# Performance work log

Measured on AMD Instinct MI355X. Metric: run time of the kernel, lower is better.

## Reference

```python
import jax, jax.numpy as jnp
import numpy as np

B = 2048      # env batch (graphs)
A = 8         # agents per graph (fully connected)
N = B * A     # total nodes
DIN = 192     # raw obs dim
HD = 256      # h_dim (base MLP)
MD = 256      # mem_dim (GRU)
GD = 128      # gnn_dim (per-head GATv2 out, concat=False -> head mean)
H = 4         # GAT heads
NA = 20       # n_actions
ED = 3        # edge_dim


def setup_inputs() -> dict:
    key = jax.random.key(0)
    ks = jax.random.split(key, 16)
    # fully-connected directed graph per group of A agents, no self loops
    s, d = np.meshgrid(np.arange(A), np.arange(A), indexing='ij')
    mask = s != d
    s = s[mask]; d = d[mask]                     # [A*(A-1)]
    off = (np.arange(B) * A)[:, None]
    src = (off + s[None, :]).reshape(-1)
    dst = (off + d[None, :]).reshape(-1)
    edge_index = jnp.asarray(np.stack([src, dst]), dtype=jnp.int32)  # [2, E]
    E = src.shape[0]
    p = lambda k, sh: jax.random.normal(ks[k], sh, jnp.float32) * 0.02
    return {
        'inputs': jax.random.normal(ks[0], (N, DIN), jnp.float32),
        'hidden_states': jax.random.normal(ks[1], (N, MD), jnp.float32) * 0.1,
        'edge_index': edge_index,
        'edge_attr': jax.random.uniform(ks[2], (E, ED), jnp.float32),
        # base MLP (2 layers: Linear+ReLU+LayerNorm)
        'W1': p(3, (DIN, HD)), 'b1': jnp.zeros(HD), 'g1': jnp.ones(HD), 'be1': jnp.zeros(HD),
        'W2': p(4, (HD, HD)),  'b2': jnp.zeros(HD), 'g2': jnp.ones(HD), 'be2': jnp.zeros(HD),
        # GRUCell
        'Wih': p(5, (3 * MD, HD)), 'Whh': p(6, (3 * MD, MD)),
        'bih': jnp.zeros(3 * MD), 'bhh': jnp.zeros(3 * MD),
        # GATv2Conv (edge_dim=3, heads=4, concat=False, residual)
        'Wl': p(7, (MD, H * GD)), 'bl': jnp.zeros(H * GD),
        'Wr': p(8, (MD, H * GD)), 'br': jnp.zeros(H * GD),
        'att': p(9, (H, GD)),
        'We': p(10, (ED, H * GD)),
        'Wres': p(11, (MD, GD)),
        'bg': jnp.zeros(GD),
        # head: LayerNorm + Linear
        'lng': jnp.ones(GD), 'lnb': jnp.zeros(GD),
        'Wout': p(12, (GD, NA)), 'bout': jnp.zeros(NA),
    }


def _ln(x, g, b):
    mu = jnp.mean(x, -1, keepdims=True)
    xc = x - mu
    v = jnp.mean(xc * xc, -1, keepdims=True)
    return xc * jax.lax.rsqrt(v + 1e-5) * g + b


def _fwd(inputs, hidden_states, edge_attr, edge_index,
         W1, b1, g1, be1, W2, b2, g2, be2,
         Wih, Whh, bih, bhh,
         Wl, bl, Wr, br, att, We, Wres, bg,
         lng, lnb, Wout, bout):
    src, dst = edge_index[0], edge_index[1]
    # ---- base MLP encode ----
    x = _ln(jax.nn.relu(inputs @ W1 + b1), g1, be1)
    x = _ln(jax.nn.relu(x @ W2 + b2), g2, be2)          # [N, HD]
    # ---- SimpleConv(aggr='mean', combine_root='self_loop') ----
    s = jax.ops.segment_sum(x[src], dst, num_segments=N) + x
    deg = jax.ops.segment_sum(jnp.ones(src.shape[0], x.dtype), dst, num_segments=N) + 1.0
    x = s / deg[:, None]                                 # [N, HD]
    # ---- GRUCell ----
    gi = x @ Wih.T + bih
    gh = hidden_states @ Whh.T + bhh
    ir, iz, inn = jnp.split(gi, 3, -1)
    hr, hz, hn = jnp.split(gh, 3, -1)
    r = jax.nn.sigmoid(ir + hr)
    z = jax.nn.sigmoid(iz + hz)
    n = jnp.tanh(inn + r * hn)
    h = (1.0 - z) * n + z * hidden_states                # [N, MD]
    # ---- GATv2Conv (add self loops, edge_attr fill='mean') ----
    loop = jnp.arange(N, dtype=src.dtype)
    sf = jnp.concatenate([src, loop])
    df = jnp.concatenate([dst, loop])
    ea = jnp.concatenate([edge_attr, jnp.broadcast_to(edge_attr.mean(0), (N, ED))], 0)
    xl = (h @ Wl + bl).reshape(N, H, GD)
    xr = (h @ Wr + br).reshape(N, H, GD)
    m = xl[sf] + xr[df] + (ea @ We).reshape(-1, H, GD)   # [Ef, H, GD]
    m = jnp.where(m > 0, m, 0.2 * m)                     # leaky_relu(0.2)
    logits = jnp.einsum('ehc,hc->eh', m, att)            # [Ef, H]
    mx = jax.ops.segment_max(logits, df, num_segments=N)
    ex = jnp.exp(logits - mx[df])
    den = jax.ops.segment_sum(ex, df, num_segments=N)
    alpha = ex / (den[df] + 1e-16)                       # segment softmax
    out = jax.ops.segment_sum(xl[sf] * alpha[..., None], df, num_segments=N)
    out = out.mean(1) + h @ Wres + bg                    # head mean + residual + bias
    zg = jax.nn.relu(out)                                # [N, GD]
    # ---- action head ----
    q = _ln(zg, lng, lnb) @ Wout + bout                  # [N, NA]
    return q, h


def reference(inputs, hidden_states, edge_index, edge_attr,
              W1, b1, g1, be1, W2, b2, g2, be2,
              Wih, Whh, bih, bhh,
              Wl, bl, Wr, br, att, We, Wres, bg,
              lng, lnb, Wout, bout):
    return _fwd(inputs, hidden_states, edge_attr, edge_index,
                W1, b1, g1, be1, W2, b2, g2, be2,
                Wih, Whh, bih, bhh,
                Wl, bl, Wr, br, att, We, Wres, bg,
                lng, lnb, Wout, bout)
```

## Files before the change

### kernel.cpp

```cpp
#include <hip/hip_runtime.h>
#include <hip/hip_bf16.h>

constexpr int NB  = 2048;
constexpr int AG  = 8;
constexpr int NN  = NB * AG;
constexpr int DIN = 192;
constexpr int HD  = 256;
constexpr int MD  = 256;
constexpr int GD  = 128;
constexpr int NA  = 20;
constexpr int NE  = NB * AG * (AG - 1);

typedef __attribute__((ext_vector_type(8))) short bfrag8;
typedef __attribute__((ext_vector_type(4))) short sfrag4;
typedef __attribute__((ext_vector_type(4))) float f32x4;

#define MFMA16(a, b, c) __builtin_amdgcn_mfma_f32_16x16x32_bf16((a), (b), (c), 0, 0, 0)

__device__ __forceinline__ float bf2f(__hip_bfloat16 x) { return __bfloat162float(x); }
__device__ __forceinline__ __hip_bfloat16 f2bf(float x) { return __float2bfloat16(x); }
__device__ __forceinline__ short f2bs(float x) {
    __hip_bfloat16 b = __float2bfloat16(x);
    return *reinterpret_cast<short*>(&b);
}
__device__ __forceinline__ bfrag8 ldf(const __hip_bfloat16* p) { return *(const bfrag8*)p; }
__device__ __forceinline__ bfrag8 ldf32(const float* p) {
    const f32x4 a = *(const f32x4*)p;
    const f32x4 b = *(const f32x4*)(p + 4);
    bfrag8 r;
    r[0] = f2bs(a[0]); r[1] = f2bs(a[1]); r[2] = f2bs(a[2]); r[3] = f2bs(a[3]);
    r[4] = f2bs(b[0]); r[5] = f2bs(b[1]); r[6] = f2bs(b[2]); r[7] = f2bs(b[3]);
    return r;
}
__device__ __forceinline__ float sigmf(float x) { return 1.f / (1.f + __expf(-x)); }
__device__ __forceinline__ float blo(unsigned u) { return __uint_as_float(u << 16); }
__device__ __forceinline__ float bhi(unsigned u) { return __uint_as_float(u & 0xffff0000u); }

__global__ __launch_bounds__(256) void k_prep(
    const float* __restrict__ W1, const float* __restrict__ W2,
    const float* __restrict__ Wih, const float* __restrict__ Whh,
    const float* __restrict__ Wl, const float* __restrict__ bl,
    const float* __restrict__ Wr, const float* __restrict__ br,
    const float* __restrict__ Wres, const float* __restrict__ Wout,
    const float* __restrict__ ea,
    __hip_bfloat16* __restrict__ W1T, __hip_bfloat16* __restrict__ W2T,
    __hip_bfloat16* __restrict__ WihB, __hip_bfloat16* __restrict__ WhhB,
    __hip_bfloat16* __restrict__ WcatT, float* __restrict__ WoutTf,
    float* __restrict__ bcat, float* __restrict__ ea_partials)
{
    __shared__ float sw[4][3];
    const int tid = threadIdx.x;
    if (blockIdx.x >= 3151) {
        const int b = blockIdx.x - 3151;
        float a0 = 0.f, a1 = 0.f, a2 = 0.f;
#pragma unroll
        for (int k = 0; k < 7; k++) {
            int e = b * 1792 + k * 256 + tid;
            a0 += ea[e * 3 + 0];
            a1 += ea[e * 3 + 1];
            a2 += ea[e * 3 + 2];
        }
#pragma unroll
        for (int off = 1; off < 64; off <<= 1) {
            a0 += __shfl_xor(a0, off); a1 += __shfl_xor(a1, off); a2 += __shfl_xor(a2, off);
        }
        if ((tid & 63) == 0) { sw[tid >> 6][0] = a0; sw[tid >> 6][1] = a1; sw[tid >> 6][2] = a2; }
        __syncthreads();
        if (tid == 0) {
            ea_partials[b * 3 + 0] = sw[0][0] + sw[1][0] + sw[2][0] + sw[3][0];
            ea_partials[b * 3 + 1] = sw[0][1] + sw[1][1] + sw[2][1] + sw[3][1];
            ea_partials[b * 3 + 2] = sw[0][2] + sw[1][2] + sw[2][2] + sw[3][2];
        }
        return;
    }
    int i = blockIdx.x * 256 + tid;
    if (i < 49152) { int o = i / 192, c = i % 192; W1T[i] = f2bf(W1[c * 256 + o]); return; }
    i -= 49152;
    if (i < 65536) { int o = i >> 8, c = i & 255; W2T[i] = f2bf(W2[c * 256 + o]); return; }
    i -= 65536;
    if (i < 196608) { WihB[i] = f2bf(Wih[i]); return; }
    i -= 196608;
    if (i < 196608) { WhhB[i] = f2bf(Whh[i]); return; }
    i -= 196608;
    if (i < 294912) {
        int o = i >> 8, c = i & 255;
        float v;
        if (o < 512)       v = Wl[c * 512 + o];
        else if (o < 1024) v = Wr[c * 512 + (o - 512)];
        else               v = Wres[c * 128 + (o - 1024)];
        WcatT[i] = f2bf(v); return;
    }
    i -= 294912;
    if (i < 2560) { int o = i >> 7, c = i & 127; WoutTf[i] = Wout[c * 20 + o]; return; }
    i -= 2560;
    if (i < 1152) {
        float v = 0.f;
        if (i < 512) v = bl[i]; else if (i < 1024) v = br[i - 512];
        bcat[i] = v;
    }
}

__global__ __launch_bounds__(256) void k_encode(
    const float* __restrict__ in,
    const __hip_bfloat16* __restrict__ W1T,
    const float* __restrict__ b1, const float* __restrict__ g1, const float* __restrict__ be1,
    const __hip_bfloat16* __restrict__ W2T,
    const float* __restrict__ b2, const float* __restrict__ g2, const float* __restrict__ be2,
    __hip_bfloat16* __restrict__ xm)
{
    __shared__ float sf[16][257];
    __shared__ alignas(16) __hip_bfloat16 sb[16][264];
    const int tid = threadIdx.x;
    const int lane = tid & 63, w = tid >> 6;
    const int r = lane & 15, q = lane >> 4;
    const int m0 = blockIdx.x * 16;

    {
        bfrag8 af[6];
        const float* ap = in + (size_t)(m0 + r) * DIN + q * 8;
#pragma unroll
        for (int kb = 0; kb < 6; kb++) af[kb] = ldf32(ap + kb * 32);
#pragma unroll
        for (int i = 0; i < 4; i++) {
            int t = w * 4 + i;
            const __hip_bfloat16* wp = W1T + (size_t)(t * 16 + r) * DIN + q * 8;
            bfrag8 bf[6];
#pragma unroll
            for (int kb = 0; kb < 6; kb++) bf[kb] = ldf(wp + kb * 32);
            f32x4 acc = (f32x4){0.f, 0.f, 0.f, 0.f};
#pragma unroll
            for (int kb = 0; kb < 6; kb++) acc = MFMA16(af[kb], bf[kb], acc);
            int col = t * 16 + r;
            float bias = b1[col];
#pragma unroll
            for (int reg = 0; reg < 4; reg++)
                sf[q * 4 + reg][col] = fmaxf(acc[reg] + bias, 0.f);
        }
    }
    __syncthreads();
    {
        int rowi = tid >> 4, c16 = tid & 15;
        float vals[16]; float s = 0.f, s2 = 0.f;
#pragma unroll
        for (int j = 0; j < 16; j++) { float v = sf[rowi][c16 + 16 * j]; vals[j] = v; s += v; s2 += v * v; }
#pragma unroll
        for (int off = 1; off < 16; off <<= 1) { s += __shfl_xor(s, off); s2 += __shfl_xor(s2, off); }
        float mean = s * (1.f / HD);
        float var = fmaxf(s2 * (1.f / HD) - mean * mean, 0.f);
        float rs = rsqrtf(var + 1e-5f);
#pragma unroll
        for (int j = 0; j < 16; j++) {
            int col = c16 + 16 * j;
            sb[rowi][col] = f2bf((vals[j] - mean) * rs * g1[col] + be1[col]);
        }
    }
    __syncthreads();

    {
        bfrag8 af[8];
        const __hip_bfloat16* ap = &sb[r][0];
#pragma unroll
        for (int kb = 0; kb < 8; kb++) af[kb] = ldf(ap + kb * 32 + q * 8);
        float outv[4][4];
#pragma unroll
        for (int i = 0; i < 4; i++) {
            int t = w * 4 + i;
            const __hip_bfloat16* wp = W2T + (size_t)(t * 16 + r) * HD + q * 8;
            bfrag8 bf[8];
#pragma unroll
            for (int kb = 0; kb < 8; kb++) bf[kb] = ldf(wp + kb * 32);
            f32x4 acc = (f32x4){0.f, 0.f, 0.f, 0.f};
#pragma unroll
            for (int kb = 0; kb < 8; kb++) acc = MFMA16(af[kb], bf[kb], acc);
#pragma unroll
            for (int reg = 0; reg < 4; reg++) outv[i][reg] = acc[reg];
        }
        __syncthreads();
#pragma unroll
        for (int i = 0; i < 4; i++) {
            int col = (w * 4 + i) * 16 + r;
            float bias = b2[col];
#pragma unroll
            for (int reg = 0; reg < 4; reg++)
                sf[q * 4 + reg][col] = fmaxf(outv[i][reg] + bias, 0.f);
        }
    }
    __syncthreads();
    {
        int rowi = tid >> 4, c16 = tid & 15;
        float vals[16]; float s = 0.f, s2 = 0.f;
#pragma unroll
        for (int j = 0; j < 16; j++) { float v = sf[rowi][c16 + 16 * j]; vals[j] = v; s += v; s2 += v * v; }
#pragma unroll
        for (int off = 1; off < 16; off <<= 1) { s += __shfl_xor(s, off); s2 += __shfl_xor(s2, off); }
        float mean = s * (1.f / HD);
        float var = fmaxf(s2 * (1.f / HD) - mean * mean, 0.f);
        float rs = rsqrtf(var + 1e-5f);
#pragma unroll
        for (int j = 0; j < 16; j++) {
            int col = c16 + 16 * j;
            sb[rowi][col] = f2bf((vals[j] - mean) * rs * g2[col] + be2[col]);
        }
    }
    __syncthreads();
    {
        int col = tid;
        float a0 = 0.f, a1 = 0.f;
#pragma unroll
        for (int i = 0; i < 8; i++) { a0 += bf2f(sb[i][col]); a1 += bf2f(sb[8 + i][col]); }
        xm[(size_t)(2 * blockIdx.x) * HD + col] = f2bf(a0 * 0.125f);
        xm[(size_t)(2 * blockIdx.x + 1) * HD + col] = f2bf(a1 * 0.125f);
    }
}

__global__ __launch_bounds__(256) void k_gi(
    const __hip_bfloat16* __restrict__ xm,
    const __hip_bfloat16* __restrict__ WihB,
    const float* __restrict__ bih,
    float* __restrict__ gi)
{
    const int tid = threadIdx.x;
    const int lane = tid & 63, w = tid >> 6;
    const int r = lane & 15, q = lane >> 4;
    const int m0 = (blockIdx.x >> 1) * 16;
    const int t0 = (blockIdx.x & 1) * 24;

    bfrag8 af[8];
    const __hip_bfloat16* ap = xm + (size_t)(m0 + r) * MD + q * 8;
#pragma unroll
    for (int kb = 0; kb < 8; kb++) af[kb] = ldf(ap + kb * 32);
#pragma unroll
    for (int i = 0; i < 6; i++) {
        int t = t0 + w * 6 + i;
        const __hip_bfloat16* wp = WihB + (size_t)(t * 16 + r) * MD + q * 8;
        bfrag8 bf[8];
#pragma unroll
        for (int kb = 0; kb < 8; kb++) bf[kb] = ldf(wp + kb * 32);
        f32x4 acc = (f32x4){0.f, 0.f, 0.f, 0.f};
#pragma unroll
        for (int kb = 0; kb < 8; kb++) acc = MFMA16(af[kb], bf[kb], acc);
        int col = t * 16 + r;
        float bias = bih[col];
#pragma unroll
        for (int reg = 0; reg < 4; reg++) {
            int R = m0 + q * 4 + reg;
            gi[(size_t)R * 768 + col] = acc[reg] + bias;
        }
    }
}

__global__ __launch_bounds__(256, 2) void k_gruG(
    const float* __restrict__ hprev,
    const __hip_bfloat16* __restrict__ WhhB,
    const float* __restrict__ bhh,
    const float* __restrict__ gi,
    float* __restrict__ hout)
{
    const int tid = threadIdx.x;
    const int lane = tid & 63, w = tid >> 6;
    const int r = lane & 15, q = lane >> 4;
    const int m0 = (blockIdx.x >> 2) * 128;
    const int cg = (blockIdx.x & 3) * 64;

    bfrag8 afr[2][8];
#pragma unroll
    for (int t = 0; t < 2; t++) {
        const float* ap = hprev + (size_t)(m0 + (w * 2 + t) * 16 + r) * MD + q * 8;
#pragma unroll
        for (int kb = 0; kb < 8; kb++) afr[t][kb] = ldf32(ap + kb * 32);
    }
    f32x4 acc[2][12];
#pragma unroll
    for (int t = 0; t < 2; t++)
#pragma unroll
        for (int n = 0; n < 12; n++) acc[t][n] = (f32x4){0.f, 0.f, 0.f, 0.f};

#pragma unroll
    for (int kb = 0; kb < 8; kb++) {
        bfrag8 bfB[12];
#pragma unroll
        for (int g = 0; g < 3; g++)
#pragma unroll
            for (int nj = 0; nj < 4; nj++)
                bfB[g * 4 + nj] = ldf(WhhB + (size_t)(g * 256 + cg + nj * 16 + r) * MD
                                      + kb * 32 + q * 8);
#pragma unroll
        for (int t = 0; t < 2; t++)
#pragma unroll
            for (int n = 0; n < 12; n++)
                acc[t][n] = MFMA16(bfB[n], afr[t][kb], acc[t][n]);
    }

#pragma unroll
    for (int t = 0; t < 2; t++) {
        int node = m0 + (w * 2 + t) * 16 + r;
        const float* gir = gi + (size_t)(node >> 3) * 768;
#pragma unroll
        for (int nj = 0; nj < 4; nj++) {
            int c = cg + nj * 16 + q * 4;
            f32x4 gR = *(const f32x4*)&gir[c];
            f32x4 gZ = *(const f32x4*)&gir[256 + c];
            f32x4 gN = *(const f32x4*)&gir[512 + c];
            f32x4 bR = *(const f32x4*)&bhh[c];
            f32x4 bZ = *(const f32x4*)&bhh[256 + c];
            f32x4 bN = *(const f32x4*)&bhh[512 + c];
            f32x4 hp = *(const f32x4*)&hprev[(size_t)node * MD + c];
            f32x4 hv;
#pragma unroll
            for (int reg = 0; reg < 4; reg++) {
                float rr = sigmf(gR[reg] + acc[t][0 + nj][reg] + bR[reg]);
                float zz = sigmf(gZ[reg] + acc[t][4 + nj][reg] + bZ[reg]);
                float nn = tanhf(gN[reg] + rr * (acc[t][8 + nj][reg] + bN[reg]));
                hv[reg] = (1.f - zz) * nn + zz * hp[reg];
            }
            *(f32x4*)&hout[(size_t)node * MD + c] = hv;
        }
    }
}

__global__ __launch_bounds__(256, 2) void k_xlr(
    const float* __restrict__ h,
    const __hip_bfloat16* __restrict__ WcatT,
    const float* __restrict__ bcat,
    __hip_bfloat16* __restrict__ xlr)
{
    const int tid = threadIdx.x;
    const int lane = tid & 63, w = tid >> 6;
    const int r = lane & 15, q = lane >> 4;
    const int m0 = (blockIdx.x / 9) * 128;
    const int nb = (blockIdx.x % 9) * 128;

    bfrag8 afr[2][8];
#pragma unroll
    for (int t = 0; t < 2; t++) {
        const float* ap = h + (size_t)(m0 + (w * 2 + t) * 16 + r) * MD + q * 8;
#pragma unroll
        for (int kb = 0; kb < 8; kb++) afr[t][kb] = ldf32(ap + kb * 32);
    }
    f32x4 acc[2][8];
#pragma unroll
    for (int t = 0; t < 2; t++)
#pragma unroll
        for (int n = 0; n < 8; n++) acc[t][n] = (f32x4){0.f, 0.f, 0.f, 0.f};

#pragma unroll
    for (int kb = 0; kb < 8; kb++) {
        bfrag8 bfB[8];
#pragma unroll
        for (int nj = 0; nj < 8; nj++)
            bfB[nj] = ldf(WcatT + (size_t)(nb + nj * 16 + r) * MD + kb * 32 + q * 8);
#pragma unroll
        for (int t = 0; t < 2; t++)
#pragma unroll
            for (int n = 0; n < 8; n++)
                acc[t][n] = MFMA16(bfB[n], afr[t][kb], acc[t][n]);
    }

#pragma unroll
    for (int t = 0; t < 2; t++) {
        int node = m0 + (w * 2 + t) * 16 + r;
#pragma unroll
        for (int nj = 0; nj < 8; nj++) {
            int fb = nb + nj * 16 + q * 4;
            sfrag4 pk;
#pragma unroll
            for (int reg = 0; reg < 4; reg++)
                pk[reg] = f2bs(acc[t][nj][reg] + bcat[fb + reg]);
            *(sfrag4*)&xlr[(size_t)node * 1152 + fb] = pk;
        }
    }
}

__global__ __launch_bounds__(256) void k_gat(
    const __hip_bfloat16* __restrict__ xlr,
    const float* __restrict__ ea,
    const float* __restrict__ ea_partials,
    const float* __restrict__ att,
    const float* __restrict__ We,
    const float* __restrict__ bg,
    const float* __restrict__ lng, const float* __restrict__ lnb,
    const float* __restrict__ WoutTf,
    const float* __restrict__ bout,
    float* __restrict__ qout)
{
    __shared__ alignas(16) __hip_bfloat16 sx[16][1160];
    __shared__ alignas(16) float szg[16][136];
    __shared__ float slog[2][4][8][8];
    __shared__ float smean[4];
    const int tid = threadIdx.x;
    const int lane = tid & 63, w = tid >> 6;
    const int r = lane & 15, q = lane >> 4;
    const int m0 = blockIdx.x * 16;

    if (tid < 3) {
        float s = 0.f;
        for (int i = 0; i < 64; i++) s += ea_partials[i * 3 + tid];
        smean[tid] = s * (1.f / NE);
    }
    for (int idx = tid; idx < 2304; idx += 256) {
        int row = idx / 144, off = (idx % 144) * 8;
        *(uint4*)&sx[row][off] = *(const uint4*)&xlr[(size_t)(m0 + row) * 1152 + off];
    }

    float vea[2][3];
    {
        int l = (lane < 56) ? lane : 0;
#pragma unroll
        for (int g = 0; g < 2; g++) {
            const float* ep = ea + (size_t)((blockIdx.x * 2 + g) * 56 + l) * 3;
            vea[g][0] = ep[0]; vea[g][1] = ep[1]; vea[g][2] = ep[2];
        }
    }
    __syncthreads();
    const float em0 = smean[0], em1 = smean[1], em2 = smean[2];

    {
        const int li = lane & 31, half = lane >> 5;
#pragma unroll
        for (int t = 0; t < 2; t++) {
            const int combo = w * 2 + t;
            const int gg = combo >> 2, hh = combo & 3;
            const f32x4 va  = *(const f32x4*)&att[hh * 128 + li * 4];
            const f32x4 vw0 = *(const f32x4*)&We[0 * 512 + hh * 128 + li * 4];
            const f32x4 vw1 = *(const f32x4*)&We[1 * 512 + hh * 128 + li * 4];
            const f32x4 vw2 = *(const f32x4*)&We[2 * 512 + hh * 128 + li * 4];
            float at0 = va[0],  at1 = va[1],  at2 = va[2],  at3 = va[3];
            float w00 = vw0[0], w01 = vw0[1], w02 = vw0[2], w03 = vw0[3];
            float w10 = vw1[0], w11 = vw1[1], w12 = vw1[2], w13 = vw1[3];
            float w20 = vw2[0], w21 = vw2[1], w22 = vw2[2], w23 = vw2[3];
            float ve0 = vea[gg][0], ve1 = vea[gg][1], ve2 = vea[gg][2];
            float xv[4][4];
#pragma unroll
            for (int sh2 = 0; sh2 < 4; sh2++) {
                int sL = sh2 * 2 + half;
                uint2 uxl = *(const uint2*)&sx[gg * 8 + sL][hh * 128 + li * 4];
                xv[sh2][0] = blo(uxl.x); xv[sh2][1] = bhi(uxl.x);
                xv[sh2][2] = blo(uxl.y); xv[sh2][3] = bhi(uxl.y);
            }
            float mylog = 0.f;
#pragma unroll
            for (int d = 0; d < 8; d++) {
                uint2 uxr = *(const uint2*)&sx[gg * 8 + d][512 + hh * 128 + li * 4];
                float xr0 = blo(uxr.x), xr1 = bhi(uxr.x), xr2 = blo(uxr.y), xr3 = bhi(uxr.y);
#pragma unroll
                for (int sh2 = 0; sh2 < 4; sh2++) {
                    int sL = sh2 * 2 + half;
                    int el = sL * 7 + d - (d > sL ? 1 : 0);
                    float e0 = __shfl(ve0, el), e1 = __shfl(ve1, el), e2 = __shfl(ve2, el);
                    bool slf = (sL == d);
                    e0 = slf ? em0 : e0; e1 = slf ? em1 : e1; e2 = slf ? em2 : e2;
                    float p, m;
                    m = fmaf(e2, w20, fmaf(e1, w10, fmaf(e0, w00, xv[sh2][0]))) + xr0;
                    m = fmaxf(m, 0.2f * m); p = m * at0;
                    m = fmaf(e2, w21, fmaf(e1, w11, fmaf(e0, w01, xv[sh2][1]))) + xr1;
                    m = fmaxf(m, 0.2f * m); p = fmaf(m, at1, p);
                    m = fmaf(e2, w22, fmaf(e1, w12, fmaf(e0, w02, xv[sh2][2]))) + xr2;
                    m = fmaxf(m, 0.2f * m); p = fmaf(m, at2, p);
                    m = fmaf(e2, w23, fmaf(e1, w13, fmaf(e0, w03, xv[sh2][3]))) + xr3;
                    m = fmaxf(m, 0.2f * m); p = fmaf(m, at3, p);
                    p += __shfl_xor(p, 1);  p += __shfl_xor(p, 2);  p += __shfl_xor(p, 4);
                    p += __shfl_xor(p, 8);  p += __shfl_xor(p, 16);
                    float got = __shfl(p, ((lane & 1) << 5) | li);
                    bool want = ((lane >> 3) == d) && (((lane & 7) >> 1) == sh2);
                    mylog = want ? got : mylog;
                }
            }
            ((float*)&slog[gg][hh][0][0])[lane] = mylog;
        }
    }
    __syncthreads();

    if (tid < 64) {
        int sg = tid >> 5, sh2 = (tid >> 3) & 3, d = tid & 7;
        float* L = &slog[sg][sh2][d][0];
        float mx = L[0];
#pragma unroll
        for (int s = 1; s < 8; s++) mx = fmaxf(mx, L[s]);
        float ex[8]; float den = 0.f;
#pragma unroll
        for (int s = 0; s < 8; s++) { ex[s] = __expf(L[s] - mx); den += ex[s]; }
        float inv = 1.f / (den + 1e-16f);
#pragma unroll
        for (int s = 0; s < 8; s++) L[s] = ex[s] * inv;
    }
    __syncthreads();

    {
        f32x4 acc0 = (f32x4){0.f, 0.f, 0.f, 0.f};
        f32x4 acc1 = (f32x4){0.f, 0.f, 0.f, 0.f};
        const int ggr = r >> 3, dr = r & 7;
#pragma unroll
        for (int ah = 0; ah < 4; ah++) {
            bfrag8 afA;
#pragma unroll
            for (int j = 0; j < 8; j++) {
                int k = q * 8 + j;
                float v = 0.f;
                if (k < 16) {
                    int ggk = k >> 3, s = k & 7;
                    if (ggk == ggr) v = slog[ggk][ah][dr][s];
                }
                afA[j] = f2bs(v);
            }
#pragma unroll
            for (int j2 = 0; j2 < 2; j2++) {
                int chunk = w * 2 + j2;
                bfrag8 bfB;
#pragma unroll
                for (int j = 0; j < 8; j++) {
                    int k = (q * 8 + j) & 15;
                    bfB[j] = *(const short*)&sx[k][ah * 128 + chunk * 16 + r];
                }
                if (j2 == 0) acc0 = MFMA16(afA, bfB, acc0);
                else         acc1 = MFMA16(afA, bfB, acc1);
            }
        }
#pragma unroll
        for (int j2 = 0; j2 < 2; j2++) {
            f32x4 a = j2 ? acc1 : acc0;
            int c = (w * 2 + j2) * 16 + r;
            float bgc = bg[c];
#pragma unroll
            for (int reg = 0; reg < 4; reg++) {
                int row = q * 4 + reg;
                float o = a[reg] * 0.25f + bf2f(sx[row][1024 + c]) + bgc;
                szg[row][c] = fmaxf(o, 0.f);
            }
        }
    }
    __syncthreads();

    {
        int row = tid >> 4, j = tid & 15;
        float v[8]; float s = 0.f, s2 = 0.f;
#pragma unroll
        for (int cj = 0; cj < 8; cj++) { v[cj] = szg[row][j + 16 * cj]; s += v[cj]; s2 += v[cj] * v[cj]; }
#pragma unroll
        for (int off = 1; off < 16; off <<= 1) { s += __shfl_xor(s, off); s2 += __shfl_xor(s2, off); }
        float mean = s * (1.f / GD);
        float var = fmaxf(s2 * (1.f / GD) - mean * mean, 0.f);
        float rs = rsqrtf(var + 1e-5f);
#pragma unroll
        for (int cj = 0; cj < 8; cj++) {
            int c = j + 16 * cj;
            szg[row][c] = (v[cj] - mean) * rs * lng[c] + lnb[c];
        }
    }
    __syncthreads();

    {
        int row = tid >> 4, j = tid & 15;
        for (int jj = j; jj < NA; jj += 16) {
            float a = bout[jj];
            const float* wo = WoutTf + jj * 128;
#pragma unroll
            for (int c4 = 0; c4 < 32; c4++) {
                f32x4 z = *(const f32x4*)&szg[row][c4 * 4];
                const f32x4 wv = *(const f32x4*)&wo[c4 * 4];
                a = fmaf(z[0], wv[0], a); a = fmaf(z[1], wv[1], a);
                a = fmaf(z[2], wv[2], a); a = fmaf(z[3], wv[3], a);
            }
            qout[(size_t)(m0 + row) * NA + jj] = a;
        }
    }
}

extern "C" void kernel_launch(void* const* d_in, const int* in_sizes, int n_in,
                              void* d_out, int out_size, void* d_ws, size_t ws_size,
                              hipStream_t stream) {
    const float* inp   = (const float*)d_in[0];
    const float* hid   = (const float*)d_in[1];
    const float* eatt  = (const float*)d_in[3];
    const float* W1    = (const float*)d_in[4];
    const float* b1    = (const float*)d_in[5];
    const float* g1    = (const float*)d_in[6];
    const float* be1   = (const float*)d_in[7];
    const float* W2    = (const float*)d_in[8];
    const float* b2    = (const float*)d_in[9];
    const float* g2    = (const float*)d_in[10];
    const float* be2   = (const float*)d_in[11];
    const float* Wih   = (const float*)d_in[12];
    const float* Whh   = (const float*)d_in[13];
    const float* bih   = (const float*)d_in[14];
    const float* bhh   = (const float*)d_in[15];
    const float* Wl    = (const float*)d_in[16];
    const float* bl    = (const float*)d_in[17];
    const float* Wr    = (const float*)d_in[18];
    const float* br    = (const float*)d_in[19];
    const float* att   = (const float*)d_in[20];
    const float* We    = (const float*)d_in[21];
    const float* Wres  = (const float*)d_in[22];
    const float* bg    = (const float*)d_in[23];
    const float* lng   = (const float*)d_in[24];
    const float* lnb   = (const float*)d_in[25];
    const float* Wout  = (const float*)d_in[26];
    const float* bout  = (const float*)d_in[27];

    float* qout = (float*)d_out;
    float* hout = (float*)d_out + (size_t)NN * NA;

    char* ws = (char*)d_ws;
    float*           ea_partials = (float*)ws;
    __hip_bfloat16*  xm    = (__hip_bfloat16*)(ws + 2048);
    float*           gi    = (float*)(ws + 1050624);
    __hip_bfloat16*  W1T   = (__hip_bfloat16*)(ws + 7342080);
    __hip_bfloat16*  W2T   = (__hip_bfloat16*)(ws + 7440384);
    __hip_bfloat16*  WihB  = (__hip_bfloat16*)(ws + 7571456);
    __hip_bfloat16*  WhhB  = (__hip_bfloat16*)(ws + 7964672);
    __hip_bfloat16*  WcatT = (__hip_bfloat16*)(ws + 8357888);
    float*           bcat  = (float*)(ws + 8947712);
    float*           WoutTf= (float*)(ws + 8952320);
    __hip_bfloat16*  xlr   = (__hip_bfloat16*)(ws + 8962560);

    k_prep<<<3215, 256, 0, stream>>>(W1, W2, Wih, Whh, Wl, bl, Wr, br, Wres, Wout, eatt,
                                     W1T, W2T, WihB, WhhB, WcatT, WoutTf, bcat, ea_partials);
    k_encode<<<NN / 16, 256, 0, stream>>>(inp, W1T, b1, g1, be1, W2T, b2, g2, be2, xm);
    k_gi<<<256, 256, 0, stream>>>(xm, WihB, bih, gi);
    k_gruG<<<512, 256, 0, stream>>>(hid, WhhB, bhh, gi, hout);
    k_xlr<<<1152, 256, 0, stream>>>(hout, WcatT, bcat, xlr);
    k_gat<<<NN / 16, 256, 0, stream>>>(xlr, eatt, ea_partials, att, We, bg,
                                       lng, lnb, WoutTf, bout, qout);
}
```

Measured before the change: 329.9 us.

## Restructure encoder to per-wave row tiles and widen xlr column tiles

The encoder kernel now gives each wave its own 16 rows across all 256 columns, so LayerNorm statistics are reduced in registers with shuffles. This removes the fp32 shared staging buffer and most block barriers, and the agent-mean is done with a cross-lane shuffle. Each block now processes 64 rows instead of 16, so every W1/W2 fragment it loads serves more rows. The xlr GEMM also loops over three 128-column chunks per block, reusing the A fragments loaded from h, which cuts the number of blocks and redundant loads of h. The trade-off is more registers (16 accumulators per wave) and fewer blocks, which may lower occupancy.

```diff
diff --git a/kernel.cpp b/kernel.cpp
--- a/kernel.cpp
+++ b/kernel.cpp
@@ -108,108 +108,131 @@
     const float* __restrict__ b2, const float* __restrict__ g2, const float* __restrict__ be2,
     __hip_bfloat16* __restrict__ xm)
 {
-    __shared__ float sf[16][257];
-    __shared__ alignas(16) __hip_bfloat16 sb[16][264];
+    __shared__ alignas(16) __hip_bfloat16 sb[64][264];
     const int tid = threadIdx.x;
     const int lane = tid & 63, w = tid >> 6;
     const int r = lane & 15, q = lane >> 4;
-    const int m0 = blockIdx.x * 16;
+    const int mt = blockIdx.x * 64 + w * 16;
+
+    f32x4 acc[16];
 
     {
         bfrag8 af[6];
-        const float* ap = in + (size_t)(m0 + r) * DIN + q * 8;
+        const float* ap = in + (size_t)(mt + r) * DIN + q * 8;
 #pragma unroll
         for (int kb = 0; kb < 6; kb++) af[kb] = ldf32(ap + kb * 32);
 #pragma unroll
-        for (int i = 0; i < 4; i++) {
-            int t = w * 4 + i;
-            const __hip_bfloat16* wp = W1T + (size_t)(t * 16 + r) * DIN + q * 8;
-            bfrag8 bf[6];
-#pragma unroll
-            for (int kb = 0; kb < 6; kb++) bf[kb] = ldf(wp + kb * 32);
-            f32x4 acc = (f32x4){0.f, 0.f, 0.f, 0.f};
-#pragma unroll
-            for (int kb = 0; kb < 6; kb++) acc = MFMA16(af[kb], bf[kb], acc);
+        for (int t = 0; t < 16; t++) acc[t] = (f32x4){0.f, 0.f, 0.f, 0.f};
+#pragma unroll
+        for (int kb = 0; kb < 6; kb++) {
+#pragma unroll
+            for (int half = 0; half < 2; half++) {
+                bfrag8 bfv[8];
+#pragma unroll
+                for (int j = 0; j < 8; j++)
+                    bfv[j] = ldf(W1T + (size_t)((half * 8 + j) * 16 + r) * DIN + kb * 32 + q * 8);
+#pragma unroll
+                for (int j = 0; j < 8; j++)
+                    acc[half * 8 + j] = MFMA16(af[kb], bfv[j], acc[half * 8 + j]);
+            }
+        }
+    }
+    {
+        float s[4] = {0.f, 0.f, 0.f, 0.f}, s2[4] = {0.f, 0.f, 0.f, 0.f};
+#pragma unroll
+        for (int t = 0; t < 16; t++) {
+            float bias = b1[t * 16 + r];
+#pragma unroll
+            for (int reg = 0; reg < 4; reg++) {
+                float x = fmaxf(acc[t][reg] + bias, 0.f);
+                acc[t][reg] = x; s[reg] += x; s2[reg] += x * x;
+            }
+        }
+#pragma unroll
+        for (int reg = 0; reg < 4; reg++) {
+#pragma unroll
+            for (int off = 1; off < 16; off <<= 1) {
+                s[reg] += __shfl_xor(s[reg], off);
+                s2[reg] += __shfl_xor(s2[reg], off);
+            }
+        }
+        float mean[4], rs[4];
+#pragma unroll
+        for (int reg = 0; reg < 4; reg++) {
+            mean[reg] = s[reg] * (1.f / HD);
+            float var = fmaxf(s2[reg] * (1.f / HD) - mean[reg] * mean[reg], 0.f);
+            rs[reg] = rsqrtf(var + 1e-5f);
+        }
+#pragma unroll
+        for (int t = 0; t < 16; t++) {
             int col = t * 16 + r;
-            float bias = b1[col];
+            float gg = g1[col], bb = be1[col];
 #pragma unroll
             for (int reg = 0; reg < 4; reg++)
-                sf[q * 4 + reg][col] = fmaxf(acc[reg] + bias, 0.f);
-        }
-    }
-    __syncthreads();
-    {
-        int rowi = tid >> 4, c16 = tid & 15;
-        float vals[16]; float s = 0.f, s2 = 0.f;
-#pragma unroll
-        for (int j = 0; j < 16; j++) { float v = sf[rowi][c16 + 16 * j]; vals[j] = v; s += v; s2 += v * v; }
-#pragma unroll
-        for (int off = 1; off < 16; off <<= 1) { s += __shfl_xor(s, off); s2 += __shfl_xor(s2, off); }
-        float mean = s * (1.f / HD);
-        float var = fmaxf(s2 * (1.f / HD) - mean * mean, 0.f);
-        float rs = rsqrtf(var + 1e-5f);
-#pragma unroll
-        for (int j = 0; j < 16; j++) {
-            int col = c16 + 16 * j;
-            sb[rowi][col] = f2bf((vals[j] - mean) * rs * g1[col] + be1[col]);
-        }
-    }
-    __syncthreads();
+                sb[w * 16 + q * 4 + reg][col] =
+                    f2bf((acc[t][reg] - mean[reg]) * rs[reg] * gg + bb);
+        }
+    }
 
     {
         bfrag8 af[8];
-        const __hip_bfloat16* ap = &sb[r][0];
-#pragma unroll
-        for (int kb = 0; kb < 8; kb++) af[kb] = ldf(ap + kb * 32 + q * 8);
-        float outv[4][4];
-#pragma unroll
-        for (int i = 0; i < 4; i++) {
-            int t = w * 4 + i;
-            const __hip_bfloat16* wp = W2T + (size_t)(t * 16 + r) * HD + q * 8;
-            bfrag8 bf[8];
-#pragma unroll
-            for (int kb = 0; kb < 8; kb++) bf[kb] = ldf(wp + kb * 32);
-            f32x4 acc = (f32x4){0.f, 0.f, 0.f, 0.f};
-#pragma unroll
-            for (int kb = 0; kb < 8; kb++) acc = MFMA16(af[kb], bf[kb], acc);
-#pragma unroll
-            for (int reg = 0; reg < 4; reg++) outv[i][reg] = acc[reg];
-        }
-        __syncthreads();
-#pragma unroll
-        for (int i = 0; i < 4; i++) {
-            int col = (w * 4 + i) * 16 + r;
-            float bias = b2[col];
+#pragma unroll
+        for (int kb = 0; kb < 8; kb++) af[kb] = ldf(&sb[w * 16 + r][kb * 32 + q * 8]);
+#pragma unroll
+        for (int t = 0; t < 16; t++) acc[t] = (f32x4){0.f, 0.f, 0.f, 0.f};
+#pragma unroll
+        for (int kb = 0; kb < 8; kb++) {
+#pragma unroll
+            for (int half = 0; half < 2; half++) {
+                bfrag8 bfv[8];
+#pragma unroll
+                for (int j = 0; j < 8; j++)
+                    bfv[j] = ldf(W2T + (size_t)((half * 8 + j) * 16 + r) * HD + kb * 32 + q * 8);
+#pragma unroll
+                for (int j = 0; j < 8; j++)
+                    acc[half * 8 + j] = MFMA16(af[kb], bfv[j], acc[half * 8 + j]);
+            }
+        }
+    }
+    {
+        float s[4] = {0.f, 0.f, 0.f, 0.f}, s2[4] = {0.f, 0.f, 0.f, 0.f};
+#pragma unroll
+        for (int t = 0; t < 16; t++) {
+            float bias = b2[t * 16 + r];
+#pragma unroll
+            for (int reg = 0; reg < 4; reg++) {
+                float x = fmaxf(acc[t][reg] + bias, 0.f);
+                acc[t][reg] = x; s[reg] += x; s2[reg] += x * x;
+            }
+        }
+#pragma unroll
+        for (int reg = 0; reg < 4; reg++) {
+#pragma unroll
+            for (int off = 1; off < 16; off <<= 1) {
+                s[reg] += __shfl_xor(s[reg], off);
+                s2[reg] += __shfl_xor(s2[reg], off);
+            }
+        }
+        float mean[4], rs[4];
+#pragma unroll
+        for (int reg = 0; reg < 4; reg++) {
+            mean[reg] = s[reg] * (1.f / HD);
+            float var = fmaxf(s2[reg] * (1.f / HD) - mean[reg] * mean[reg], 0.f);
+            rs[reg] = rsqrtf(var + 1e-5f);
+        }
+        const int gbase = mt >> 3;
+#pragma unroll
+        for (int t = 0; t < 16; t++) {
+            int col = t * 16 + r;
+            float gg = g2[col], bb = be2[col];
+            float gsum = 0.f;
 #pragma unroll
             for (int reg = 0; reg < 4; reg++)
-                sf[q * 4 + reg][col] = fmaxf(outv[i][reg] + bias, 0.f);
-        }
-    }
-    __syncthreads();
-    {
-        int rowi = tid >> 4, c16 = tid & 15;
-        float vals[16]; float s = 0.f, s2 = 0.f;
-#pragma unroll
-        for (int j = 0; j < 16; j++) { float v = sf[rowi][c16 + 16 * j]; vals[j] = v; s += v; s2 += v * v; }
-#pragma unroll
-        for (int off = 1; off < 16; off <<= 1) { s += __shfl_xor(s, off); s2 += __shfl_xor(s2, off); }
-        float mean = s * (1.f / HD);
-        float var = fmaxf(s2 * (1.f / HD) - mean * mean, 0.f);
-        float rs = rsqrtf(var + 1e-5f);
-#pragma unroll
-        for (int j = 0; j < 16; j++) {
-            int col = c16 + 16 * j;
-            sb[rowi][col] = f2bf((vals[j] - mean) * rs * g2[col] + be2[col]);
-        }
-    }
-    __syncthreads();
-    {
-        int col = tid;
-        float a0 = 0.f, a1 = 0.f;
-#pragma unroll
-        for (int i = 0; i < 8; i++) { a0 += bf2f(sb[i][col]); a1 += bf2f(sb[8 + i][col]); }
-        xm[(size_t)(2 * blockIdx.x) * HD + col] = f2bf(a0 * 0.125f);
-        xm[(size_t)(2 * blockIdx.x + 1) * HD + col] = f2bf(a1 * 0.125f);
+                gsum += (acc[t][reg] - mean[reg]) * rs[reg] * gg + bb;
+            gsum += __shfl_xor(gsum, 16);
+            if (q == 0)      xm[(size_t)gbase * HD + col]       = f2bf(gsum * 0.125f);
+            else if (q == 2) xm[(size_t)(gbase + 1) * HD + col] = f2bf(gsum * 0.125f);
+        }
     }
 }
 
@@ -327,8 +350,8 @@
     const int tid = threadIdx.x;
     const int lane = tid & 63, w = tid >> 6;
     const int r = lane & 15, q = lane >> 4;
-    const int m0 = (blockIdx.x / 9) * 128;
-    const int nb = (blockIdx.x % 9) * 128;
+    const int m0 = (blockIdx.x / 3) * 128;
+    const int nb0 = (blockIdx.x % 3) * 384;
 
     bfrag8 afr[2][8];
 #pragma unroll
@@ -337,36 +360,38 @@
 #pragma unroll
         for (int kb = 0; kb < 8; kb++) afr[t][kb] = ldf32(ap + kb * 32);
     }
-    f32x4 acc[2][8];
-#pragma unroll
-    for (int t = 0; t < 2; t++)
-#pragma unroll
-        for (int n = 0; n < 8; n++) acc[t][n] = (f32x4){0.f, 0.f, 0.f, 0.f};
-
-#pragma unroll
-    for (int kb = 0; kb < 8; kb++) {
-        bfrag8 bfB[8];
-#pragma unroll
-        for (int nj = 0; nj < 8; nj++)
-            bfB[nj] = ldf(WcatT + (size_t)(nb + nj * 16 + r) * MD + kb * 32 + q * 8);
+#pragma unroll
+    for (int chunk = 0; chunk < 3; chunk++) {
+        const int nb = nb0 + chunk * 128;
+        f32x4 acc[2][8];
 #pragma unroll
         for (int t = 0; t < 2; t++)
 #pragma unroll
-            for (int n = 0; n < 8; n++)
-                acc[t][n] = MFMA16(bfB[n], afr[t][kb], acc[t][n]);
-    }
-
-#pragma unroll
-    for (int t = 0; t < 2; t++) {
-        int node = m0 + (w * 2 + t) * 16 + r;
-#pragma unroll
-        for (int nj = 0; nj < 8; nj++) {
-            int fb = nb + nj * 16 + q * 4;
-            sfrag4 pk;
-#pragma unroll
-            for (int reg = 0; reg < 4; reg++)
-                pk[reg] = f2bs(acc[t][nj][reg] + bcat[fb + reg]);
-            *(sfrag4*)&xlr[(size_t)node * 1152 + fb] = pk;
+            for (int n = 0; n < 8; n++) acc[t][n] = (f32x4){0.f, 0.f, 0.f, 0.f};
+#pragma unroll
+        for (int kb = 0; kb < 8; kb++) {
+            bfrag8 bfB[8];
+#pragma unroll
+            for (int nj = 0; nj < 8; nj++)
+                bfB[nj] = ldf(WcatT + (size_t)(nb + nj * 16 + r) * MD + kb * 32 + q * 8);
+#pragma unroll
+            for (int t = 0; t < 2; t++)
+#pragma unroll
+                for (int n = 0; n < 8; n++)
+                    acc[t][n] = MFMA16(bfB[n], afr[t][kb], acc[t][n]);
+        }
+#pragma unroll
+        for (int t = 0; t < 2; t++) {
+            int node = m0 + (w * 2 + t) * 16 + r;
+#pragma unroll
+            for (int nj = 0; nj < 8; nj++) {
+                int fb = nb + nj * 16 + q * 4;
+                sfrag4 pk;
+#pragma unroll
+                for (int reg = 0; reg < 4; reg++)
+                    pk[reg] = f2bs(acc[t][nj][reg] + bcat[fb + reg]);
+                *(sfrag4*)&xlr[(size_t)node * 1152 + fb] = pk;
+            }
         }
     }
 }
@@ -614,10 +639,10 @@
 
     k_prep<<<3215, 256, 0, stream>>>(W1, W2, Wih, Whh, Wl, bl, Wr, br, Wres, Wout, eatt,
                                      W1T, W2T, WihB, WhhB, WcatT, WoutTf, bcat, ea_partials);
-    k_encode<<<NN / 16, 256, 0, stream>>>(inp, W1T, b1, g1, be1, W2T, b2, g2, be2, xm);
+    k_encode<<<NN / 64, 256, 0, stream>>>(inp, W1T, b1, g1, be1, W2T, b2, g2, be2, xm);
     k_gi<<<256, 256, 0, stream>>>(xm, WihB, bih, gi);
     k_gruG<<<512, 256, 0, stream>>>(hid, WhhB, bhh, gi, hout);
-    k_xlr<<<1152, 256, 0, stream>>>(hout, WcatT, bcat, xlr);
+    k_xlr<<<384, 256, 0, stream>>>(hout, WcatT, bcat, xlr);
     k_gat<<<NN / 16, 256, 0, stream>>>(xlr, eatt, ea_partials, att, We, bg,
                                        lng, lnb, WoutTf, bout, qout);
 }
```

After: 416.2 us. +26.2%, slower.

## Remap GEMM block indices across XCDs and shrink GAT blocks to one graph

Applied to the files above, without the earlier changes.

The GRU and xlr GEMM kernels now derive their row and column tile indices from a permuted block ID. Consecutive row tiles land on different dispatch slices while the column tiles of one row tile stay on the same XCD, which should improve L2 reuse of the shared A rows. The GAT kernel now processes one 8-node graph per block instead of two, doubling the grid and halving LDS per block. Each wave handles one head, with a matching XCD-aware block-to-graph permutation. This raises occupancy and parallelism, but half the MFMA rows and half the threads in the layernorm and output stages now sit idle.

```diff
diff --git a/kernel.cpp b/kernel.cpp
--- a/kernel.cpp
+++ b/kernel.cpp
@@ -259,8 +259,10 @@
     const int tid = threadIdx.x;
     const int lane = tid & 63, w = tid >> 6;
     const int r = lane & 15, q = lane >> 4;
-    const int m0 = (blockIdx.x >> 2) * 128;
-    const int cg = (blockIdx.x & 3) * 64;
+    const int b = blockIdx.x, y = b & 7, k = b >> 3;
+    const int rt = y + 8 * (k >> 2);
+    const int m0 = rt * 128;
+    const int cg = (k & 3) * 64;
 
     bfrag8 afr[2][8];
 #pragma unroll
@@ -327,8 +329,9 @@
     const int tid = threadIdx.x;
     const int lane = tid & 63, w = tid >> 6;
     const int r = lane & 15, q = lane >> 4;
-    const int m0 = (blockIdx.x / 9) * 128;
-    const int nb = (blockIdx.x % 9) * 128;
+    const int b = blockIdx.x, y = b & 7, k = b >> 3;
+    const int m0 = (y + 8 * (k / 9)) * 128;
+    const int nb = (k % 9) * 128;
 
     bfrag8 afr[2][8];
 #pragma unroll
@@ -383,96 +386,91 @@
     const float* __restrict__ bout,
     float* __restrict__ qout)
 {
-    __shared__ alignas(16) __hip_bfloat16 sx[16][1160];
-    __shared__ alignas(16) float szg[16][136];
-    __shared__ float slog[2][4][8][8];
+    __shared__ alignas(16) __hip_bfloat16 sx[8][1160];
+    __shared__ alignas(16) float szg[8][136];
+    __shared__ float slog[4][8][8];
     __shared__ float smean[4];
     const int tid = threadIdx.x;
     const int lane = tid & 63, w = tid >> 6;
     const int r = lane & 15, q = lane >> 4;
-    const int m0 = blockIdx.x * 16;
+    const int b = blockIdx.x;
+    const int l = ((b & 7) << 3) + ((b >> 3) & 7) + (b & ~63);
+    const int g = l;
+    const int m0 = g * 8;
 
     if (tid < 3) {
         float s = 0.f;
         for (int i = 0; i < 64; i++) s += ea_partials[i * 3 + tid];
         smean[tid] = s * (1.f / NE);
     }
-    for (int idx = tid; idx < 2304; idx += 256) {
+    for (int idx = tid; idx < 1152; idx += 256) {
         int row = idx / 144, off = (idx % 144) * 8;
         *(uint4*)&sx[row][off] = *(const uint4*)&xlr[(size_t)(m0 + row) * 1152 + off];
     }
 
-    float vea[2][3];
-    {
-        int l = (lane < 56) ? lane : 0;
-#pragma unroll
-        for (int g = 0; g < 2; g++) {
-            const float* ep = ea + (size_t)((blockIdx.x * 2 + g) * 56 + l) * 3;
-            vea[g][0] = ep[0]; vea[g][1] = ep[1]; vea[g][2] = ep[2];
-        }
+    float ve0, ve1, ve2;
+    {
+        int ll = (lane < 56) ? lane : 0;
+        const float* ep = ea + (size_t)(g * 56 + ll) * 3;
+        ve0 = ep[0]; ve1 = ep[1]; ve2 = ep[2];
     }
     __syncthreads();
     const float em0 = smean[0], em1 = smean[1], em2 = smean[2];
 
     {
         const int li = lane & 31, half = lane >> 5;
-#pragma unroll
-        for (int t = 0; t < 2; t++) {
-            const int combo = w * 2 + t;
-            const int gg = combo >> 2, hh = combo & 3;
-            const f32x4 va  = *(const f32x4*)&att[hh * 128 + li * 4];
-            const f32x4 vw0 = *(const f32x4*)&We[0 * 512 + hh * 128 + li * 4];
-            const f32x4 vw1 = *(const f32x4*)&We[1 * 512 + hh * 128 + li * 4];
-            const f32x4 vw2 = *(const f32x4*)&We[2 * 512 + hh * 128 + li * 4];
-            float at0 = va[0],  at1 = va[1],  at2 = va[2],  at3 = va[3];
-            float w00 = vw0[0], w01 = vw0[1], w02 = vw0[2], w03 = vw0[3];
-            float w10 = vw1[0], w11 = vw1[1], w12 = vw1[2], w13 = vw1[3];
-            float w20 = vw2[0], w21 = vw2[1], w22 = vw2[2], w23 = vw2[3];
-            float ve0 = vea[gg][0], ve1 = vea[gg][1], ve2 = vea[gg][2];
-            float xv[4][4];
+        const int hh = w;
+        const f32x4 va  = *(const f32x4*)&att[hh * 128 + li * 4];
+        const f32x4 vw0 = *(const f32x4*)&We[0 * 512 + hh * 128 + li * 4];
+        const f32x4 vw1 = *(const f32x4*)&We[1 * 512 + hh * 128 + li * 4];
+        const f32x4 vw2 = *(const f32x4*)&We[2 * 512 + hh * 128 + li * 4];
+        float at0 = va[0],  at1 = va[1],  at2 = va[2],  at3 = va[3];
+        float w00 = vw0[0], w01 = vw0[1], w02 = vw0[2], w03 = vw0[3];
+        float w10 = vw1[0], w11 = vw1[1], w12 = vw1[2], w13 = vw1[3];
+        float w20 = vw2[0], w21 = vw2[1], w22 = vw2[2], w23 = vw2[3];
+        float xv[4][4];
+#pragma unroll
+        for (int sh2 = 0; sh2 < 4; sh2++) {
+            int sL = sh2 * 2 + half;
+            uint2 uxl = *(const uint2*)&sx[sL][hh * 128 + li * 4];
+            xv[sh2][0] = blo(uxl.x); xv[sh2][1] = bhi(uxl.x);
+            xv[sh2][2] = blo(uxl.y); xv[sh2][3] = bhi(uxl.y);
+        }
+        float mylog = 0.f;
+#pragma unroll
+        for (int d = 0; d < 8; d++) {
+            uint2 uxr = *(const uint2*)&sx[d][512 + hh * 128 + li * 4];
+            float xr0 = blo(uxr.x), xr1 = bhi(uxr.x), xr2 = blo(uxr.y), xr3 = bhi(uxr.y);
 #pragma unroll
             for (int sh2 = 0; sh2 < 4; sh2++) {
                 int sL = sh2 * 2 + half;
-                uint2 uxl = *(const uint2*)&sx[gg * 8 + sL][hh * 128 + li * 4];
-                xv[sh2][0] = blo(uxl.x); xv[sh2][1] = bhi(uxl.x);
-                xv[sh2][2] = blo(uxl.y); xv[sh2][3] = bhi(uxl.y);
+                int el = sL * 7 + d - (d > sL ? 1 : 0);
+                float e0 = __shfl(ve0, el), e1 = __shfl(ve1, el), e2 = __shfl(ve2, el);
+                bool slf = (sL == d);
+                e0 = slf ? em0 : e0; e1 = slf ? em1 : e1; e2 = slf ? em2 : e2;
+                float p, m;
+                m = fmaf(e2, w20, fmaf(e1, w10, fmaf(e0, w00, xv[sh2][0]))) + xr0;
+                m = fmaxf(m, 0.2f * m); p = m * at0;
+                m = fmaf(e2, w21, fmaf(e1, w11, fmaf(e0, w01, xv[sh2][1]))) + xr1;
+                m = fmaxf(m, 0.2f * m); p = fmaf(m, at1, p);
+                m = fmaf(e2, w22, fmaf(e1, w12, fmaf(e0, w02, xv[sh2][2]))) + xr2;
+                m = fmaxf(m, 0.2f * m); p = fmaf(m, at2, p);
+                m = fmaf(e2, w23, fmaf(e1, w13, fmaf(e0, w03, xv[sh2][3]))) + xr3;
+                m = fmaxf(m, 0.2f * m); p = fmaf(m, at3, p);
+                p += __shfl_xor(p, 1);  p += __shfl_xor(p, 2);  p += __shfl_xor(p, 4);
+                p += __shfl_xor(p, 8);  p += __shfl_xor(p, 16);
+                float got = __shfl(p, ((lane & 1) << 5) | li);
+                bool want = ((lane >> 3) == d) && (((lane & 7) >> 1) == sh2);
+                mylog = want ? got : mylog;
             }
-            float mylog = 0.f;
-#pragma unroll
-            for (int d = 0; d < 8; d++) {
-                uint2 uxr = *(const uint2*)&sx[gg * 8 + d][512 + hh * 128 + li * 4];
-                float xr0 = blo(uxr.x), xr1 = bhi(uxr.x), xr2 = blo(uxr.y), xr3 = bhi(uxr.y);
-#pragma unroll
-                for (int sh2 = 0; sh2 < 4; sh2++) {
-                    int sL = sh2 * 2 + half;
-                    int el = sL * 7 + d - (d > sL ? 1 : 0);
-                    float e0 = __shfl(ve0, el), e1 = __shfl(ve1, el), e2 = __shfl(ve2, el);
-                    bool slf = (sL == d);
-                    e0 = slf ? em0 : e0; e1 = slf ? em1 : e1; e2 = slf ? em2 : e2;
-                    float p, m;
-                    m = fmaf(e2, w20, fmaf(e1, w10, fmaf(e0, w00, xv[sh2][0]))) + xr0;
-                    m = fmaxf(m, 0.2f * m); p = m * at0;
-                    m = fmaf(e2, w21, fmaf(e1, w11, fmaf(e0, w01, xv[sh2][1]))) + xr1;
-                    m = fmaxf(m, 0.2f * m); p = fmaf(m, at1, p);
-                    m = fmaf(e2, w22, fmaf(e1, w12, fmaf(e0, w02, xv[sh2][2]))) + xr2;
-                    m = fmaxf(m, 0.2f * m); p = fmaf(m, at2, p);
-                    m = fmaf(e2, w23, fmaf(e1, w13, fmaf(e0, w03, xv[sh2][3]))) + xr3;
-                    m = fmaxf(m, 0.2f * m); p = fmaf(m, at3, p);
-                    p += __shfl_xor(p, 1);  p += __shfl_xor(p, 2);  p += __shfl_xor(p, 4);
-                    p += __shfl_xor(p, 8);  p += __shfl_xor(p, 16);
-                    float got = __shfl(p, ((lane & 1) << 5) | li);
-                    bool want = ((lane >> 3) == d) && (((lane & 7) >> 1) == sh2);
-                    mylog = want ? got : mylog;
-                }
-            }
-            ((float*)&slog[gg][hh][0][0])[lane] = mylog;
-        }
-    }
-    __syncthreads();
-
-    if (tid < 64) {
-        int sg = tid >> 5, sh2 = (tid >> 3) & 3, d = tid & 7;
-        float* L = &slog[sg][sh2][d][0];
+        }
+        ((float*)&slog[hh][0][0])[lane] = mylog;
+    }
+    __syncthreads();
+
+    if (tid < 32) {
+        int sh2 = tid >> 3, d = tid & 7;
+        float* L = &slog[sh2][d][0];
         float mx = L[0];
 #pragma unroll
         for (int s = 1; s < 8; s++) mx = fmaxf(mx, L[s]);
@@ -488,18 +486,13 @@
     {
         f32x4 acc0 = (f32x4){0.f, 0.f, 0.f, 0.f};
         f32x4 acc1 = (f32x4){0.f, 0.f, 0.f, 0.f};
-        const int ggr = r >> 3, dr = r & 7;
 #pragma unroll
         for (int ah = 0; ah < 4; ah++) {
             bfrag8 afA;
 #pragma unroll
             for (int j = 0; j < 8; j++) {
                 int k = q * 8 + j;
-                float v = 0.f;
-                if (k < 16) {
-                    int ggk = k >> 3, s = k & 7;
-                    if (ggk == ggr) v = slog[ggk][ah][dr][s];
-                }
+                float v = (k < 8 && r < 8) ? slog[ah][r][k] : 0.f;
                 afA[j] = f2bs(v);
             }
 #pragma unroll
@@ -508,7 +501,7 @@
                 bfrag8 bfB;
 #pragma unroll
                 for (int j = 0; j < 8; j++) {
-                    int k = (q * 8 + j) & 15;
+                    int k = (q * 8 + j) & 7;
                     bfB[j] = *(const short*)&sx[k][ah * 128 + chunk * 16 + r];
                 }
                 if (j2 == 0) acc0 = MFMA16(afA, bfB, acc0);
@@ -523,14 +516,16 @@
 #pragma unroll
             for (int reg = 0; reg < 4; reg++) {
                 int row = q * 4 + reg;
-                float o = a[reg] * 0.25f + bf2f(sx[row][1024 + c]) + bgc;
-                szg[row][c] = fmaxf(o, 0.f);
+                if (row < 8) {
+                    float o = a[reg] * 0.25f + bf2f(sx[row][1024 + c]) + bgc;
+                    szg[row][c] = fmaxf(o, 0.f);
+                }
             }
         }
     }
     __syncthreads();
 
-    {
+    if (tid < 128) {
         int row = tid >> 4, j = tid & 15;
         float v[8]; float s = 0.f, s2 = 0.f;
 #pragma unroll
@@ -548,7 +543,7 @@
     }
     __syncthreads();
 
-    {
+    if (tid < 128) {
         int row = tid >> 4, j = tid & 15;
         for (int jj = j; jj < NA; jj += 16) {
             float a = bout[jj];
@@ -618,6 +613,6 @@
     k_gi<<<256, 256, 0, stream>>>(xm, WihB, bih, gi);
     k_gruG<<<512, 256, 0, stream>>>(hid, WhhB, bhh, gi, hout);
     k_xlr<<<1152, 256, 0, stream>>>(hout, WcatT, bcat, xlr);
-    k_gat<<<NN / 16, 256, 0, stream>>>(xlr, eatt, ea_partials, att, We, bg,
-                                       lng, lnb, WoutTf, bout, qout);
-}
+    k_gat<<<NB, 256, 0, stream>>>(xlr, eatt, ea_partials, att, We, bg,
+                                  lng, lnb, WoutTf, bout, qout);
+}
```

After: 342.3 us. +3.8%, slower.
